# Performance work log

Hardware: AMD Instinct MI355X
Metric: run time of the kernel (lower is better)

The kernel has to match this reference:

```python
import jax, jax.numpy as jnp
import numpy as np
from jax import lax

KH = 5
KW = 5


def dwconv3x3(x, w, b):
    # depthwise 3x3, padding 1; w: (C,1,3,3), b: (C,)
    C = x.shape[1]
    y = lax.conv_general_dilated(x, w, (1, 1), ((1, 1), (1, 1)),
                                 feature_group_count=C,
                                 dimension_numbers=('NCHW', 'OIHW', 'NCHW'))
    return y + b[None, :, None, None]


def conv3x3(x, w, b):
    y = lax.conv_general_dilated(x, w, (1, 1), ((1, 1), (1, 1)),
                                 dimension_numbers=('NCHW', 'OIHW', 'NCHW'))
    return y + b[None, :, None, None]


def resize_bilinear_ac(x, H, W):
    # bilinear, align_corners=True (matches F.interpolate(..., align_corners=True))
    N, C, h, w = x.shape
    ys = jnp.linspace(0.0, h - 1.0, H)
    xs = jnp.linspace(0.0, w - 1.0, W)
    y0 = jnp.floor(ys).astype(jnp.int32)
    x0 = jnp.floor(xs).astype(jnp.int32)
    y1 = jnp.clip(y0 + 1, 0, h - 1)
    x1 = jnp.clip(x0 + 1, 0, w - 1)
    wy = (ys - y0)[None, None, :, None]
    wx = (xs - x0)[None, None, None, :]
    rows = x[:, :, y0, :] * (1.0 - wy) + x[:, :, y1, :] * wy  # (N,C,H,w)
    out = rows[:, :, :, x0] * (1.0 - wx) + rows[:, :, :, x1] * wx  # (N,C,H,W)
    return out


def unfold_kxk(x, kH, kW):
    # torch.nn.Unfold(kernel=(kH,kW), padding=(kH//2,kW//2)) reshaped to (N,C,kH*kW,H,W)
    N, C, H, W = x.shape
    ph, pw = kH // 2, kW // 2
    xp = jnp.pad(x, ((0, 0), (0, 0), (ph, ph), (pw, pw)))
    patches = [xp[:, :, i:i + H, j:j + W] for i in range(kH) for j in range(kW)]
    return jnp.stack(patches, axis=2)  # (N,C,kH*kW,H,W), row-major window order


def setup_inputs() -> dict:
    key = jax.random.key(0)
    ks = jax.random.split(key, 11)
    N, C, H, W = 2, 128, 128, 128
    s = 1.0 / np.sqrt(9.0)
    return {
        'hr_feat': jax.random.normal(ks[0], (N, C, H, W), jnp.float32),
        'lr_feat': jax.random.normal(ks[1], (N, C, H // 2, W // 2), jnp.float32),
        'wq': jax.random.normal(ks[2], (C, 1, 3, 3), jnp.float32) * s,
        'bq': jax.random.normal(ks[3], (C,), jnp.float32) * 0.02,
        'wk': jax.random.normal(ks[4], (C, 1, 3, 3), jnp.float32) * s,
        'bk': jax.random.normal(ks[5], (C,), jnp.float32) * 0.02,
        'wv': jax.random.normal(ks[6], (C, 1, 3, 3), jnp.float32) * s,
        'bv': jax.random.normal(ks[7], (C,), jnp.float32) * 0.02,
        'wa': jax.random.normal(ks[8], (2, 2 * C, 3, 3), jnp.float32) * (1.0 / np.sqrt(9.0 * 2 * C)),
        'ba': jax.random.normal(ks[9], (2,), jnp.float32) * 0.02,
    }


def reference(hr_feat, lr_feat, wq, bq, wk, bk, wv, bv, wa, ba):
    N, C, H, W = hr_feat.shape
    lr_up = resize_bilinear_ac(lr_feat, H, W)
    hr_value = dwconv3x3(hr_feat, wv, bv)
    hr_key = dwconv3x3(hr_feat, wk, bk)
    lr_query = dwconv3x3(lr_up, wq, bq)
    fused = jnp.concatenate([lr_query, hr_key], axis=1)
    dyn = jax.nn.sigmoid(conv3x3(fused, wa, ba))  # (N,2,H,W)
    k_unf = unfold_kxk(hr_key, KH, KW)            # (N,C,K,H,W)
    sim = jnp.einsum('nchw,nckhw->nkhw', lr_query, k_unf)
    weight = jax.nn.softmax(sim, axis=1)          # softmax over window K
    v_unf = unfold_kxk(hr_value, KH, KW)
    attn = dyn[:, 0:1] * jnp.einsum('nckhw,nkhw->nchw', v_unf, weight)
    attn = attn + dyn[:, 1:2] * hr_value
    return lr_up + attn
```

## Files before the change

kernel.cpp:

```cpp
#include <hip/hip_runtime.h>
#include <hip/hip_fp16.h>
#include <math.h>

constexpr int C  = 128;
constexpr int H  = 128;
constexpr int Wd = 128;
constexpr int HW = H * Wd;
constexpr int LH = 64, LW = 64;
constexpr int CP = 64;

constexpr int KRW = 136;
constexpr int KPLANE = 132 * KRW;
constexpr int QRW = 136;
constexpr int QPLANE = 130 * QRW;
constexpr int KSZ = 2 * CP * KPLANE;
constexpr int QSZ = 2 * CP * QPLANE;
constexpr int LSZ = 2 * CP * HW;
constexpr int WAHSZ = 2304;

typedef _Float16 __attribute__((ext_vector_type(2))) v2h;

#if __has_builtin(__builtin_amdgcn_fdot2)
#define DOT2(a, b, c) __builtin_amdgcn_fdot2((a), (b), (c), false)
#else
#define DOT2(a, b, c) ((c) + (float)(a).x * (float)(b).x + (float)(a).y * (float)(b).y)
#endif

struct __attribute__((packed, aligned(4)))  f4u { float x, y, z, w; };
struct __attribute__((packed, aligned(4)))  f4p { v2h a, b, c, d; };
struct __attribute__((packed, aligned(8)))  h2x2 { v2h a, b; };
struct __attribute__((packed, aligned(16))) h4 { v2h a, b, c, d; };

__device__ __forceinline__ v2h pack2(float a, float b) {
  v2h r; r.x = (_Float16)a; r.y = (_Float16)b; return r;
}

__global__ __launch_bounds__(256) void k_pre(
    const float* __restrict__ hr, const float* __restrict__ lr,
    const float* __restrict__ wq, const float* __restrict__ bq,
    const float* __restrict__ wk, const float* __restrict__ bk,
    const float* __restrict__ wv, const float* __restrict__ bv,
    const float* __restrict__ wa,
    v2h* __restrict__ qpad, v2h* __restrict__ kpad, v2h* __restrict__ vpad,
    v2h* __restrict__ lrup, v2h* __restrict__ zgapA, v2h* __restrict__ zgapB,
    v2h* __restrict__ wah)
{
  const int B   = blockIdx.x;
  const int tid = threadIdx.x;
  const int t   = B * 256 + tid;
  const int q   = B & 7;
  const int m   = B >> 3;
  const int j   = (q << 1) | (m & 1);
  const int ncp = m >> 1;
  const int x4  = tid & 31;
  const int y   = (j << 3) | ((tid >> 5) & 7);
  const int x   = x4 * 4;
  const int cp  = ncp & (CP - 1);
  const int n   = ncp >> 6;
  const int c0  = cp * 2;
  const v2h hz  = pack2(0.f, 0.f);
  h4 Z; Z.a = hz; Z.b = hz; Z.c = hz; Z.d = hz;

  if (t < WAHSZ) {
    const int cpw = t / 36, r = t - cpw * 36;
    const int o = r / 18, s2 = (r - o * 18) / 9, tap = r - o * 18 - s2 * 9;
    const int c = s2 * 128 + 2 * cpw;
    wah[t] = pack2(wa[(o * 256 + c) * 9 + tap], wa[(o * 256 + c + 1) * 9 + tap]);
  }

  float ko[2][4], vo[2][4];
#pragma unroll
  for (int cc = 0; cc < 2; cc++) {
    const int c = c0 + cc;
    const float* hp = hr + (n * C + c) * HW;
    const float* wkc = wk + c * 9;
    const float* wvc = wv + c * 9;
    const float bkc = bk[c], bvc = bv[c];
#pragma unroll
    for (int jj = 0; jj < 4; jj++) { ko[cc][jj] = bkc; vo[cc][jj] = bvc; }
#pragma unroll
    for (int r = 0; r < 3; r++) {
      const int gy = y + r - 1;
      const bool okr = (gy >= 0) && (gy < H);
      const int gyc = min(max(gy, 0), H - 1);
      const float* rp = hp + gyc * Wd;
      const f4u mm = *(const f4u*)(rp + x);
      const float lft = rp[max(x - 1, 0)];
      const float rgt = rp[min(x + 4, Wd - 1)];
      float h[6];
      h[0] = (okr && x > 0) ? lft : 0.f;
      h[1] = okr ? mm.x : 0.f;  h[2] = okr ? mm.y : 0.f;
      h[3] = okr ? mm.z : 0.f;  h[4] = okr ? mm.w : 0.f;
      h[5] = (okr && x + 4 < Wd) ? rgt : 0.f;
#pragma unroll
      for (int dj = 0; dj < 3; dj++) {
        const float a = wkc[r * 3 + dj], b = wvc[r * 3 + dj];
#pragma unroll
        for (int jj = 0; jj < 4; jj++) {
          ko[cc][jj] += a * h[jj + dj];
          vo[cc][jj] += b * h[jj + dj];
        }
      }
    }
  }

  v2h* kr = kpad + ncp * KPLANE + (y + 2) * KRW + 4 + x;
  v2h* vr = vpad + ncp * KPLANE + (y + 2) * KRW + 4 + x;
  {
    h4 K4; K4.a = pack2(ko[0][0], ko[1][0]); K4.b = pack2(ko[0][1], ko[1][1]);
           K4.c = pack2(ko[0][2], ko[1][2]); K4.d = pack2(ko[0][3], ko[1][3]);
    h4 V4; V4.a = pack2(vo[0][0], vo[1][0]); V4.b = pack2(vo[0][1], vo[1][1]);
           V4.c = pack2(vo[0][2], vo[1][2]); V4.d = pack2(vo[0][3], vo[1][3]);
    *(h4*)(kr) = K4;
    *(h4*)(vr) = V4;
  }

  const float s = 63.0f / 127.0f;

  float rwm[3][3]; int rA[3];
  {
    int ry0[3]; float wyv[3]; bool okr[3];
#pragma unroll
    for (int r = 0; r < 3; r++) {
      const int gy = y + r - 1;
      okr[r] = (gy >= 0) && (gy < H);
      const int gyc = min(max(gy, 0), H - 1);
      const float fy = gyc * s;
      const int y0 = (int)fy;
      ry0[r] = y0;
      wyv[r] = fy - y0;
    }
    const int Y = ry0[0];
#pragma unroll
    for (int tt = 0; tt < 3; tt++) rA[tt] = min(Y + tt, LH - 1) * LW;
#pragma unroll
    for (int r = 0; r < 3; r++) {
      const int i0 = ry0[r] - Y;
      const int i1 = min(ry0[r] + 1, LH - 1) - Y;
#pragma unroll
      for (int tt = 0; tt < 3; tt++) {
        const float w = ((tt == i0) ? (1.f - wyv[r]) : 0.f)
                      + ((tt == i1) ? wyv[r] : 0.f);
        rwm[r][tt] = okr[r] ? w : 0.f;
      }
    }
  }

  float cwm[6][5]; int XB;
  {
    int cx0[6]; float wxv[6]; bool okc[6];
#pragma unroll
    for (int jj = 0; jj < 6; jj++) {
      const int gx = x + jj - 1;
      okc[jj] = (gx >= 0) && (gx < Wd);
      const int gxc = min(max(gx, 0), Wd - 1);
      const float fx = gxc * s;
      const int x0 = (int)fx;
      cx0[jj] = x0;
      wxv[jj] = fx - x0;
    }
    XB = min(cx0[0], LW - 5);
#pragma unroll
    for (int jj = 0; jj < 6; jj++) {
      const int i0 = cx0[jj] - XB;
      const int i1 = min(cx0[jj] + 1, LW - 1) - XB;
#pragma unroll
      for (int u = 0; u < 5; u++) {
        const float w = ((u == i0) ? (1.f - wxv[jj]) : 0.f)
                      + ((u == i1) ? wxv[jj] : 0.f);
        cwm[jj][u] = okc[jj] ? w : 0.f;
      }
    }
  }

  float qo[2][4], up[2][4];
#pragma unroll
  for (int cc = 0; cc < 2; cc++) {
    const int c = c0 + cc;
    const float* lp = lr + (n * C + c) * (LH * LW);
    const float* wqc = wq + c * 9;
    const float bqc = bq[c];
#pragma unroll
    for (int jj = 0; jj < 4; jj++) qo[cc][jj] = bqc;

    float R[3][5];
#pragma unroll
    for (int tt = 0; tt < 3; tt++) {
      const f4u mm = *(const f4u*)(lp + rA[tt] + XB);
      R[tt][0] = mm.x; R[tt][1] = mm.y; R[tt][2] = mm.z; R[tt][3] = mm.w;
      R[tt][4] = lp[rA[tt] + XB + 4];
    }

    float yi[3][5];
#pragma unroll
    for (int r = 0; r < 3; r++)
#pragma unroll
      for (int u = 0; u < 5; u++)
        yi[r][u] = rwm[r][0] * R[0][u] + rwm[r][1] * R[1][u]
                 + rwm[r][2] * R[2][u];

#pragma unroll
    for (int r = 0; r < 3; r++) {
      float row[6];
#pragma unroll
      for (int jj = 0; jj < 6; jj++)
        row[jj] = cwm[jj][0] * yi[r][0] + cwm[jj][1] * yi[r][1]
               + cwm[jj][2] * yi[r][2] + cwm[jj][3] * yi[r][3]
               + cwm[jj][4] * yi[r][4];
#pragma unroll
      for (int dj = 0; dj < 3; dj++) {
        const float a = wqc[r * 3 + dj];
#pragma unroll
        for (int jj = 0; jj < 4; jj++) qo[cc][jj] += a * row[jj + dj];
      }
      if (r == 1) {
        up[cc][0] = row[1]; up[cc][1] = row[2];
        up[cc][2] = row[3]; up[cc][3] = row[4];
      }
    }
  }

  {
    h4 U;
    U.a = pack2(up[0][0], up[1][0]); U.b = pack2(up[0][1], up[1][1]);
    U.c = pack2(up[0][2], up[1][2]); U.d = pack2(up[0][3], up[1][3]);
    *(h4*)(lrup + ncp * HW + y * Wd + x) = U;
  }
  v2h* qr = qpad + ncp * QPLANE + (y + 1) * QRW + 4 + x;
  {
    h4 Q4; Q4.a = pack2(qo[0][0], qo[1][0]); Q4.b = pack2(qo[0][1], qo[1][1]);
           Q4.c = pack2(qo[0][2], qo[1][2]); Q4.d = pack2(qo[0][3], qo[1][3]);
    *(h4*)(qr) = Q4;
  }

  if (x4 == 0) {
    *(h4*)(kr - 4) = Z; *(h4*)(vr - 4) = Z; *(h4*)(qr - 4) = Z;
  }
  if (x4 == 31) {
    *(h4*)(kr + 4) = Z; *(h4*)(vr + 4) = Z; *(h4*)(qr + 4) = Z;
  }
  if (y == 0) {
    v2h* kz = kpad + ncp * KPLANE;
    v2h* vz = vpad + ncp * KPLANE;
    v2h* qz = qpad + ncp * QPLANE;
    *(h4*)(kz + 4 + x) = Z; *(h4*)(kz + KRW + 4 + x) = Z;
    *(h4*)(vz + 4 + x) = Z; *(h4*)(vz + KRW + 4 + x) = Z;
    *(h4*)(qz + 4 + x) = Z;
    if (x4 == 0) {
      *(h4*)(kz) = Z; *(h4*)(kz + KRW) = Z;
      *(h4*)(vz) = Z; *(h4*)(vz + KRW) = Z;
      *(h4*)(qz) = Z;
    }
    if (x4 == 31) {
      *(h4*)(kz + 132) = Z; *(h4*)(kz + KRW + 132) = Z;
      *(h4*)(vz + 132) = Z; *(h4*)(vz + KRW + 132) = Z;
      *(h4*)(qz + 132) = Z;
    }
  }
  if (y == 127) {
    v2h* kz = kpad + ncp * KPLANE + 130 * KRW;
    v2h* vz = vpad + ncp * KPLANE + 130 * KRW;
    v2h* qz = qpad + ncp * QPLANE + 129 * QRW;
    *(h4*)(kz + 4 + x) = Z; *(h4*)(kz + KRW + 4 + x) = Z;
    *(h4*)(vz + 4 + x) = Z; *(h4*)(vz + KRW + 4 + x) = Z;
    *(h4*)(qz + 4 + x) = Z;
    if (x4 == 0) {
      *(h4*)(kz) = Z; *(h4*)(kz + KRW) = Z;
      *(h4*)(vz) = Z; *(h4*)(vz + KRW) = Z;
      *(h4*)(qz) = Z;
    }
    if (x4 == 31) {
      *(h4*)(kz + 132) = Z; *(h4*)(kz + KRW + 132) = Z;
      *(h4*)(vz + 132) = Z; *(h4*)(vz + KRW + 132) = Z;
      *(h4*)(qz + 132) = Z;
    }
  }
  if (t < 256) zgapA[t] = hz;
  if (t < 4)   zgapB[t] = hz;
}

#define DECLK(P, kp) \
  const f4p P##A0 = *(const f4p*)(kp); \
  const f4p P##A1 = *(const f4p*)((kp) + KRW); \
  const f4p P##A2 = *(const f4p*)((kp) + 2 * KRW); \
  const f4p P##A3 = *(const f4p*)((kp) + 3 * KRW); \
  const f4p P##A4 = *(const f4p*)((kp) + 4 * KRW); \
  const v2h P##b0 = (kp)[4]; \
  const v2h P##b1 = (kp)[KRW + 4]; \
  const v2h P##b2 = (kp)[2 * KRW + 4]; \
  const v2h P##b3 = (kp)[3 * KRW + 4]; \
  const v2h P##b4 = (kp)[4 * KRW + 4];

#define DECLQ(P, qp) \
  const f4p P##Q0 = *(const f4p*)(qp); \
  const f4p P##Q1 = *(const f4p*)((qp) + QRW); \
  const f4p P##Q2 = *(const f4p*)((qp) + 2 * QRW);

#define SIM25(P, qc) \
  sim[0]  = DOT2(qc, P##A0.a, sim[0]);  sim[1]  = DOT2(qc, P##A0.b, sim[1]); \
  sim[2]  = DOT2(qc, P##A0.c, sim[2]);  sim[3]  = DOT2(qc, P##A0.d, sim[3]); \
  sim[4]  = DOT2(qc, P##b0,   sim[4]); \
  sim[5]  = DOT2(qc, P##A1.a, sim[5]);  sim[6]  = DOT2(qc, P##A1.b, sim[6]); \
  sim[7]  = DOT2(qc, P##A1.c, sim[7]);  sim[8]  = DOT2(qc, P##A1.d, sim[8]); \
  sim[9]  = DOT2(qc, P##b1,   sim[9]); \
  sim[10] = DOT2(qc, P##A2.a, sim[10]); sim[11] = DOT2(qc, P##A2.b, sim[11]); \
  sim[12] = DOT2(qc, P##A2.c, sim[12]); sim[13] = DOT2(qc, P##A2.d, sim[13]); \
  sim[14] = DOT2(qc, P##b2,   sim[14]); \
  sim[15] = DOT2(qc, P##A3.a, sim[15]); sim[16] = DOT2(qc, P##A3.b, sim[16]); \
  sim[17] = DOT2(qc, P##A3.c, sim[17]); sim[18] = DOT2(qc, P##A3.d, sim[18]); \
  sim[19] = DOT2(qc, P##b3,   sim[19]); \
  sim[20] = DOT2(qc, P##A4.a, sim[20]); sim[21] = DOT2(qc, P##A4.b, sim[21]); \
  sim[22] = DOT2(qc, P##A4.c, sim[22]); sim[23] = DOT2(qc, P##A4.d, sim[23]); \
  sim[24] = DOT2(qc, P##b4,   sim[24]);

#define GATE(P, wp) { \
  const v2h q3_[9] = {P##Q0.a, P##Q0.b, P##Q0.c, P##Q1.a, P##Q1.b, P##Q1.c, \
                      P##Q2.a, P##Q2.b, P##Q2.c}; \
  const v2h k3_[9] = {P##A1.b, P##A1.c, P##A1.d, P##A2.b, P##A2.c, P##A2.d, \
                      P##A3.b, P##A3.c, P##A3.d}; \
  _Pragma("unroll") \
  for (int tp = 0; tp < 9; tp++) { \
    d0a = DOT2((wp)[tp],      q3_[tp], d0a); \
    d0a = DOT2((wp)[9 + tp],  k3_[tp], d0a); \
    d1a = DOT2((wp)[18 + tp], q3_[tp], d1a); \
    d1a = DOT2((wp)[27 + tp], k3_[tp], d1a); \
  } }

#define EPI(P, ci) { \
  v2h accA = wpk[0] * P##A0.a; \
  accA += wpk[1]  * P##A0.b;  accA += wpk[2]  * P##A0.c; \
  accA += wpk[3]  * P##A0.d;  accA += wpk[4]  * P##b0; \
  v2h accB = wpk[5] * P##A1.a; \
  accB += wpk[6]  * P##A1.b;  accB += wpk[7]  * P##A1.c; \
  accB += wpk[8]  * P##A1.d;  accB += wpk[9]  * P##b1; \
  accA += wpk[10] * P##A2.a;  accA += wpk[11] * P##A2.b; \
  accA += wpk[12] * P##A2.c;  accA += wpk[13] * P##A2.d; \
  accA += wpk[14] * P##b2; \
  accB += wpk[15] * P##A3.a;  accB += wpk[16] * P##A3.b; \
  accB += wpk[17] * P##A3.c;  accB += wpk[18] * P##A3.d; \
  accB += wpk[19] * P##b3; \
  accA += wpk[20] * P##A4.a;  accA += wpk[21] * P##A4.b; \
  accA += wpk[22] * P##A4.c;  accA += wpk[23] * P##A4.d; \
  accA += wpk[24] * P##b4; \
  const float acc0 = (float)accA.x + (float)accB.x; \
  const float acc1 = (float)accA.y + (float)accB.y; \
  const v2h vc = P##A2.c; \
  const v2h lu = lub[(ci) * HW]; \
  float* op = opb + (ci) * 2 * HW; \
  op[0]  = (float)lu.x + g0 * acc0 + g1 * (float)vc.x; \
  op[HW] = (float)lu.y + g0 * acc1 + g1 * (float)vc.y; }

__global__ __launch_bounds__(1024, 4) void k_attn(
    const v2h* __restrict__ qpad, const v2h* __restrict__ kpad,
    const v2h* __restrict__ vpad, const v2h* __restrict__ lrup,
    const v2h* __restrict__ wah, const float* __restrict__ ba,
    float* __restrict__ outb)
{
  __shared__ float red[25 * 1024];
  __shared__ float dsh[2 * 1024];

  const int tid = threadIdx.x;
  const int px  = tid & 63;
  const int cgu = __builtin_amdgcn_readfirstlane((tid >> 6) & 7);
  const int row = __builtin_amdgcn_readfirstlane(tid >> 9);
  const int slot = blockIdx.x;
  const int xcd = slot & 7;
  const int m   = slot >> 3;
  const int y   = (xcd << 4) + ((m & 7) << 1) + row;
  const int x   = ((m >> 3) & 1) * 64 + px;
  const int n   = m >> 4;
  const int cp0 = cgu * 8;

  const float ba0 = ba[0], ba1 = ba[1];

  const v2h* kb = kpad + (n * CP + cp0) * KPLANE + y * KRW + 2 + x;
  const v2h* qb = qpad + (n * CP + cp0) * QPLANE + y * QRW + 3 + x;

  float sim[25];
#pragma unroll
  for (int k = 0; k < 25; k++) sim[k] = 0.f;
  float d0a = 0.f, d1a = 0.f;

#pragma unroll
  for (int cib = 0; cib < 8; cib += 2) {
    const v2h* kp0 = kb + cib * KPLANE;
    const v2h* kp1 = kp0 + KPLANE;
    const v2h* qp0 = qb + cib * QPLANE;
    const v2h* qp1 = qp0 + QPLANE;

    DECLK(S, kp0)
    DECLK(T, kp1)
    DECLQ(S, qp0)

    const v2h qc0 = SQ1.b;
    SIM25(S, qc0)
    GATE(S, wah + (cp0 + cib) * 36)

    DECLQ(T, qp1)
    const v2h qc1 = TQ1.b;
    SIM25(T, qc1)
    GATE(T, wah + (cp0 + cib + 1) * 36)
  }

#pragma unroll
  for (int k = 0; k < 25; k++) red[k * 1024 + tid] = sim[k];
  dsh[tid] = d0a;
  dsh[1024 + tid] = d1a;
  __syncthreads();

  {
    const int w = tid >> 6;
    for (int s = w; s < 54; s += 16) {
      if (s < 50) {
        const int k = s >> 1, r = s & 1;
        float acc = 0.f;
#pragma unroll
        for (int g = 0; g < 8; g++) acc += red[k * 1024 + r * 512 + g * 64 + px];
        red[k * 1024 + r * 512 + px] = acc;
      } else {
        const int jj = s - 50;
        const int r = jj & 1, which = jj >> 1;
        float acc = 0.f;
#pragma unroll
        for (int g = 0; g < 8; g++) acc += dsh[which * 1024 + r * 512 + g * 64 + px];
        dsh[which * 1024 + r * 512 + px] = acc;
      }
    }
  }
  __syncthreads();

  const v2h* vb = vpad + (n * CP + cp0) * KPLANE + y * KRW + 2 + x;
  const v2h* lub = lrup + (n * CP + cp0) * HW + y * Wd + x;
  float* opb = outb + (n * C + 2 * cp0) * HW + y * Wd + x;

  DECLK(VA, vb)
  DECLK(VB, vb + KPLANE)

  const int rbase = row * 512 + px;
  float w[25];
  float mx = -1e30f;
#pragma unroll
  for (int k = 0; k < 25; k++) { w[k] = red[k * 1024 + rbase]; mx = fmaxf(mx, w[k]); }
  float tot = 0.f;
#pragma unroll
  for (int k = 0; k < 25; k++) { const float e = __expf(w[k] - mx); w[k] = e; tot += e; }
  const float inv = __builtin_amdgcn_rcpf(tot);
  v2h wpk[25];
#pragma unroll
  for (int k = 0; k < 25; k++) {
    const float wf = w[k] * inv;
    wpk[k] = pack2(wf, wf);
  }
  const float g0 = __builtin_amdgcn_rcpf(1.f + __expf(-(dsh[rbase] + ba0)));
  const float g1 = __builtin_amdgcn_rcpf(1.f + __expf(-(dsh[1024 + rbase] + ba1)));

  EPI(VA, 0)
  EPI(VB, 1)

#pragma unroll
  for (int cib = 2; cib < 8; cib += 2) {
    DECLK(VC, vb + cib * KPLANE)
    DECLK(VD, vb + (cib + 1) * KPLANE)
    EPI(VC, cib)
    EPI(VD, cib + 1)
  }
}

extern "C" void kernel_launch(void* const* d_in, const int* in_sizes, int n_in,
                              void* d_out, int out_size, void* d_ws,
                              size_t ws_size, hipStream_t stream)
{
  const float* hr = (const float*)d_in[0];
  const float* lr = (const float*)d_in[1];
  const float* wq = (const float*)d_in[2];
  const float* bq = (const float*)d_in[3];
  const float* wk = (const float*)d_in[4];
  const float* bk = (const float*)d_in[5];
  const float* wv = (const float*)d_in[6];
  const float* bv = (const float*)d_in[7];
  const float* wa = (const float*)d_in[8];
  const float* ba = (const float*)d_in[9];

  float* out = (float*)d_out;
  v2h* ws2 = (v2h*)d_ws;

  v2h* kpad  = ws2;
  v2h* vpad  = kpad + KSZ;
  v2h* qpad  = vpad + KSZ;
  v2h* zgapA = qpad + QSZ;
  v2h* lrupb = zgapA + 256;
  v2h* zgapB = lrupb + LSZ;
  v2h* wahb  = zgapB + 4;

  k_pre<<<dim3(2048), dim3(256), 0, stream>>>(
      hr, lr, wq, bq, wk, bk, wv, bv, wa,
      qpad, kpad, vpad, lrupb, zgapA, zgapB, wahb);
  k_attn<<<dim3(256), dim3(1024), 0, stream>>>(
      qpad, kpad, vpad, lrupb, wahb, ba, out);
}
```

Before: 118.1 us.

## Fuse preprocessing and attention kernels into one cooperative launch with grid sync

Merges the k_pre and k_attn kernels into a single cooperative kernel. Each 1024-thread block first computes the q/k/v depthwise convs and the upsampled features for its own tile, then synchronises the whole grid before running the attention stage. This removes one kernel launch and the gap between kernels. In exchange the preprocessing stage now runs on only 256 large blocks instead of 2048 small ones, and the grid-wide barrier has its own cost.

```diff
diff --git a/kernel.cpp b/kernel.cpp
--- a/kernel.cpp
+++ b/kernel.cpp
@@ -1,6 +1,9 @@
 #include <hip/hip_runtime.h>
 #include <hip/hip_fp16.h>
+#include <hip/hip_cooperative_groups.h>
 #include <math.h>
+
+namespace cg = cooperative_groups;
 
 constexpr int C  = 128;
 constexpr int H  = 128;
@@ -28,255 +31,10 @@
 
 struct __attribute__((packed, aligned(4)))  f4u { float x, y, z, w; };
 struct __attribute__((packed, aligned(4)))  f4p { v2h a, b, c, d; };
-struct __attribute__((packed, aligned(8)))  h2x2 { v2h a, b; };
 struct __attribute__((packed, aligned(16))) h4 { v2h a, b, c, d; };
 
 __device__ __forceinline__ v2h pack2(float a, float b) {
   v2h r; r.x = (_Float16)a; r.y = (_Float16)b; return r;
-}
-
-__global__ __launch_bounds__(256) void k_pre(
-    const float* __restrict__ hr, const float* __restrict__ lr,
-    const float* __restrict__ wq, const float* __restrict__ bq,
-    const float* __restrict__ wk, const float* __restrict__ bk,
-    const float* __restrict__ wv, const float* __restrict__ bv,
-    const float* __restrict__ wa,
-    v2h* __restrict__ qpad, v2h* __restrict__ kpad, v2h* __restrict__ vpad,
-    v2h* __restrict__ lrup, v2h* __restrict__ zgapA, v2h* __restrict__ zgapB,
-    v2h* __restrict__ wah)
-{
-  const int B   = blockIdx.x;
-  const int tid = threadIdx.x;
-  const int t   = B * 256 + tid;
-  const int q   = B & 7;
-  const int m   = B >> 3;
-  const int j   = (q << 1) | (m & 1);
-  const int ncp = m >> 1;
-  const int x4  = tid & 31;
-  const int y   = (j << 3) | ((tid >> 5) & 7);
-  const int x   = x4 * 4;
-  const int cp  = ncp & (CP - 1);
-  const int n   = ncp >> 6;
-  const int c0  = cp * 2;
-  const v2h hz  = pack2(0.f, 0.f);
-  h4 Z; Z.a = hz; Z.b = hz; Z.c = hz; Z.d = hz;
-
-  if (t < WAHSZ) {
-    const int cpw = t / 36, r = t - cpw * 36;
-    const int o = r / 18, s2 = (r - o * 18) / 9, tap = r - o * 18 - s2 * 9;
-    const int c = s2 * 128 + 2 * cpw;
-    wah[t] = pack2(wa[(o * 256 + c) * 9 + tap], wa[(o * 256 + c + 1) * 9 + tap]);
-  }
-
-  float ko[2][4], vo[2][4];
-#pragma unroll
-  for (int cc = 0; cc < 2; cc++) {
-    const int c = c0 + cc;
-    const float* hp = hr + (n * C + c) * HW;
-    const float* wkc = wk + c * 9;
-    const float* wvc = wv + c * 9;
-    const float bkc = bk[c], bvc = bv[c];
-#pragma unroll
-    for (int jj = 0; jj < 4; jj++) { ko[cc][jj] = bkc; vo[cc][jj] = bvc; }
-#pragma unroll
-    for (int r = 0; r < 3; r++) {
-      const int gy = y + r - 1;
-      const bool okr = (gy >= 0) && (gy < H);
-      const int gyc = min(max(gy, 0), H - 1);
-      const float* rp = hp + gyc * Wd;
-      const f4u mm = *(const f4u*)(rp + x);
-      const float lft = rp[max(x - 1, 0)];
-      const float rgt = rp[min(x + 4, Wd - 1)];
-      float h[6];
-      h[0] = (okr && x > 0) ? lft : 0.f;
-      h[1] = okr ? mm.x : 0.f;  h[2] = okr ? mm.y : 0.f;
-      h[3] = okr ? mm.z : 0.f;  h[4] = okr ? mm.w : 0.f;
-      h[5] = (okr && x + 4 < Wd) ? rgt : 0.f;
-#pragma unroll
-      for (int dj = 0; dj < 3; dj++) {
-        const float a = wkc[r * 3 + dj], b = wvc[r * 3 + dj];
-#pragma unroll
-        for (int jj = 0; jj < 4; jj++) {
-          ko[cc][jj] += a * h[jj + dj];
-          vo[cc][jj] += b * h[jj + dj];
-        }
-      }
-    }
-  }
-
-  v2h* kr = kpad + ncp * KPLANE + (y + 2) * KRW + 4 + x;
-  v2h* vr = vpad + ncp * KPLANE + (y + 2) * KRW + 4 + x;
-  {
-    h4 K4; K4.a = pack2(ko[0][0], ko[1][0]); K4.b = pack2(ko[0][1], ko[1][1]);
-           K4.c = pack2(ko[0][2], ko[1][2]); K4.d = pack2(ko[0][3], ko[1][3]);
-    h4 V4; V4.a = pack2(vo[0][0], vo[1][0]); V4.b = pack2(vo[0][1], vo[1][1]);
-           V4.c = pack2(vo[0][2], vo[1][2]); V4.d = pack2(vo[0][3], vo[1][3]);
-    *(h4*)(kr) = K4;
-    *(h4*)(vr) = V4;
-  }
-
-  const float s = 63.0f / 127.0f;
-
-  float rwm[3][3]; int rA[3];
-  {
-    int ry0[3]; float wyv[3]; bool okr[3];
-#pragma unroll
-    for (int r = 0; r < 3; r++) {
-      const int gy = y + r - 1;
-      okr[r] = (gy >= 0) && (gy < H);
-      const int gyc = min(max(gy, 0), H - 1);
-      const float fy = gyc * s;
-      const int y0 = (int)fy;
-      ry0[r] = y0;
-      wyv[r] = fy - y0;
-    }
-    const int Y = ry0[0];
-#pragma unroll
-    for (int tt = 0; tt < 3; tt++) rA[tt] = min(Y + tt, LH - 1) * LW;
-#pragma unroll
-    for (int r = 0; r < 3; r++) {
-      const int i0 = ry0[r] - Y;
-      const int i1 = min(ry0[r] + 1, LH - 1) - Y;
-#pragma unroll
-      for (int tt = 0; tt < 3; tt++) {
-        const float w = ((tt == i0) ? (1.f - wyv[r]) : 0.f)
-                      + ((tt == i1) ? wyv[r] : 0.f);
-        rwm[r][tt] = okr[r] ? w : 0.f;
-      }
-    }
-  }
-
-  float cwm[6][5]; int XB;
-  {
-    int cx0[6]; float wxv[6]; bool okc[6];
-#pragma unroll
-    for (int jj = 0; jj < 6; jj++) {
-      const int gx = x + jj - 1;
-      okc[jj] = (gx >= 0) && (gx < Wd);
-      const int gxc = min(max(gx, 0), Wd - 1);
-      const float fx = gxc * s;
-      const int x0 = (int)fx;
-      cx0[jj] = x0;
-      wxv[jj] = fx - x0;
-    }
-    XB = min(cx0[0], LW - 5);
-#pragma unroll
-    for (int jj = 0; jj < 6; jj++) {
-      const int i0 = cx0[jj] - XB;
-      const int i1 = min(cx0[jj] + 1, LW - 1) - XB;
-#pragma unroll
-      for (int u = 0; u < 5; u++) {
-        const float w = ((u == i0) ? (1.f - wxv[jj]) : 0.f)
-                      + ((u == i1) ? wxv[jj] : 0.f);
-        cwm[jj][u] = okc[jj] ? w : 0.f;
-      }
-    }
-  }
-
-  float qo[2][4], up[2][4];
-#pragma unroll
-  for (int cc = 0; cc < 2; cc++) {
-    const int c = c0 + cc;
-    const float* lp = lr + (n * C + c) * (LH * LW);
-    const float* wqc = wq + c * 9;
-    const float bqc = bq[c];
-#pragma unroll
-    for (int jj = 0; jj < 4; jj++) qo[cc][jj] = bqc;
-
-    float R[3][5];
-#pragma unroll
-    for (int tt = 0; tt < 3; tt++) {
-      const f4u mm = *(const f4u*)(lp + rA[tt] + XB);
-      R[tt][0] = mm.x; R[tt][1] = mm.y; R[tt][2] = mm.z; R[tt][3] = mm.w;
-      R[tt][4] = lp[rA[tt] + XB + 4];
-    }
-
-    float yi[3][5];
-#pragma unroll
-    for (int r = 0; r < 3; r++)
-#pragma unroll
-      for (int u = 0; u < 5; u++)
-        yi[r][u] = rwm[r][0] * R[0][u] + rwm[r][1] * R[1][u]
-                 + rwm[r][2] * R[2][u];
-
-#pragma unroll
-    for (int r = 0; r < 3; r++) {
-      float row[6];
-#pragma unroll
-      for (int jj = 0; jj < 6; jj++)
-        row[jj] = cwm[jj][0] * yi[r][0] + cwm[jj][1] * yi[r][1]
-               + cwm[jj][2] * yi[r][2] + cwm[jj][3] * yi[r][3]
-               + cwm[jj][4] * yi[r][4];
-#pragma unroll
-      for (int dj = 0; dj < 3; dj++) {
-        const float a = wqc[r * 3 + dj];
-#pragma unroll
-        for (int jj = 0; jj < 4; jj++) qo[cc][jj] += a * row[jj + dj];
-      }
-      if (r == 1) {
-        up[cc][0] = row[1]; up[cc][1] = row[2];
-        up[cc][2] = row[3]; up[cc][3] = row[4];
-      }
-    }
-  }
-
-  {
-    h4 U;
-    U.a = pack2(up[0][0], up[1][0]); U.b = pack2(up[0][1], up[1][1]);
-    U.c = pack2(up[0][2], up[1][2]); U.d = pack2(up[0][3], up[1][3]);
-    *(h4*)(lrup + ncp * HW + y * Wd + x) = U;
-  }
-  v2h* qr = qpad + ncp * QPLANE + (y + 1) * QRW + 4 + x;
-  {
-    h4 Q4; Q4.a = pack2(qo[0][0], qo[1][0]); Q4.b = pack2(qo[0][1], qo[1][1]);
-           Q4.c = pack2(qo[0][2], qo[1][2]); Q4.d = pack2(qo[0][3], qo[1][3]);
-    *(h4*)(qr) = Q4;
-  }
-
-  if (x4 == 0) {
-    *(h4*)(kr - 4) = Z; *(h4*)(vr - 4) = Z; *(h4*)(qr - 4) = Z;
-  }
-  if (x4 == 31) {
-    *(h4*)(kr + 4) = Z; *(h4*)(vr + 4) = Z; *(h4*)(qr + 4) = Z;
-  }
-  if (y == 0) {
-    v2h* kz = kpad + ncp * KPLANE;
-    v2h* vz = vpad + ncp * KPLANE;
-    v2h* qz = qpad + ncp * QPLANE;
-    *(h4*)(kz + 4 + x) = Z; *(h4*)(kz + KRW + 4 + x) = Z;
-    *(h4*)(vz + 4 + x) = Z; *(h4*)(vz + KRW + 4 + x) = Z;
-    *(h4*)(qz + 4 + x) = Z;
-    if (x4 == 0) {
-      *(h4*)(kz) = Z; *(h4*)(kz + KRW) = Z;
-      *(h4*)(vz) = Z; *(h4*)(vz + KRW) = Z;
-      *(h4*)(qz) = Z;
-    }
-    if (x4 == 31) {
-      *(h4*)(kz + 132) = Z; *(h4*)(kz + KRW + 132) = Z;
-      *(h4*)(vz + 132) = Z; *(h4*)(vz + KRW + 132) = Z;
-      *(h4*)(qz + 132) = Z;
-    }
-  }
-  if (y == 127) {
-    v2h* kz = kpad + ncp * KPLANE + 130 * KRW;
-    v2h* vz = vpad + ncp * KPLANE + 130 * KRW;
-    v2h* qz = qpad + ncp * QPLANE + 129 * QRW;
-    *(h4*)(kz + 4 + x) = Z; *(h4*)(kz + KRW + 4 + x) = Z;
-    *(h4*)(vz + 4 + x) = Z; *(h4*)(vz + KRW + 4 + x) = Z;
-    *(h4*)(qz + 4 + x) = Z;
-    if (x4 == 0) {
-      *(h4*)(kz) = Z; *(h4*)(kz + KRW) = Z;
-      *(h4*)(vz) = Z; *(h4*)(vz + KRW) = Z;
-      *(h4*)(qz) = Z;
-    }
-    if (x4 == 31) {
-      *(h4*)(kz + 132) = Z; *(h4*)(kz + KRW + 132) = Z;
-      *(h4*)(vz + 132) = Z; *(h4*)(vz + KRW + 132) = Z;
-      *(h4*)(qz + 132) = Z;
-    }
-  }
-  if (t < 256) zgapA[t] = hz;
-  if (t < 4)   zgapB[t] = hz;
 }
 
 #define DECLK(P, kp) \
@@ -350,119 +108,359 @@
   op[0]  = (float)lu.x + g0 * acc0 + g1 * (float)vc.x; \
   op[HW] = (float)lu.y + g0 * acc1 + g1 * (float)vc.y; }
 
-__global__ __launch_bounds__(1024, 4) void k_attn(
-    const v2h* __restrict__ qpad, const v2h* __restrict__ kpad,
-    const v2h* __restrict__ vpad, const v2h* __restrict__ lrup,
-    const v2h* __restrict__ wah, const float* __restrict__ ba,
-    float* __restrict__ outb)
+__global__ __launch_bounds__(1024, 4) void k_fused(
+    const float* __restrict__ hr, const float* __restrict__ lr,
+    const float* __restrict__ wq, const float* __restrict__ bq,
+    const float* __restrict__ wk, const float* __restrict__ bk,
+    const float* __restrict__ wv, const float* __restrict__ bv,
+    const float* __restrict__ wa, const float* __restrict__ ba,
+    v2h* __restrict__ qpad, v2h* __restrict__ kpad, v2h* __restrict__ vpad,
+    v2h* __restrict__ lrup, v2h* __restrict__ zgapA, v2h* __restrict__ zgapB,
+    v2h* __restrict__ wah, float* __restrict__ outb)
 {
   __shared__ float red[25 * 1024];
   __shared__ float dsh[2 * 1024];
 
-  const int tid = threadIdx.x;
-  const int px  = tid & 63;
-  const int cgu = __builtin_amdgcn_readfirstlane((tid >> 6) & 7);
-  const int row = __builtin_amdgcn_readfirstlane(tid >> 9);
+  const int tid  = threadIdx.x;
   const int slot = blockIdx.x;
-  const int xcd = slot & 7;
-  const int m   = slot >> 3;
-  const int y   = (xcd << 4) + ((m & 7) << 1) + row;
-  const int x   = ((m >> 3) & 1) * 64 + px;
-  const int n   = m >> 4;
-  const int cp0 = cgu * 8;
-
-  const float ba0 = ba[0], ba1 = ba[1];
-
-  const v2h* kb = kpad + (n * CP + cp0) * KPLANE + y * KRW + 2 + x;
-  const v2h* qb = qpad + (n * CP + cp0) * QPLANE + y * QRW + 3 + x;
-
-  float sim[25];
-#pragma unroll
-  for (int k = 0; k < 25; k++) sim[k] = 0.f;
-  float d0a = 0.f, d1a = 0.f;
-
-#pragma unroll
-  for (int cib = 0; cib < 8; cib += 2) {
-    const v2h* kp0 = kb + cib * KPLANE;
-    const v2h* kp1 = kp0 + KPLANE;
-    const v2h* qp0 = qb + cib * QPLANE;
-    const v2h* qp1 = qp0 + QPLANE;
-
-    DECLK(S, kp0)
-    DECLK(T, kp1)
-    DECLQ(S, qp0)
-
-    const v2h qc0 = SQ1.b;
-    SIM25(S, qc0)
-    GATE(S, wah + (cp0 + cib) * 36)
-
-    DECLQ(T, qp1)
-    const v2h qc1 = TQ1.b;
-    SIM25(T, qc1)
-    GATE(T, wah + (cp0 + cib + 1) * 36)
-  }
-
-#pragma unroll
-  for (int k = 0; k < 25; k++) red[k * 1024 + tid] = sim[k];
-  dsh[tid] = d0a;
-  dsh[1024 + tid] = d1a;
-  __syncthreads();
+  const int xcd  = slot & 7;
+  const int mm_  = slot >> 3;
+  const int y0   = (xcd << 4) + ((mm_ & 7) << 1);
+  const int x0   = ((mm_ >> 3) & 1) * 64;
+  const int n    = mm_ >> 4;
 
   {
-    const int w = tid >> 6;
-    for (int s = w; s < 54; s += 16) {
-      if (s < 50) {
-        const int k = s >> 1, r = s & 1;
-        float acc = 0.f;
-#pragma unroll
-        for (int g = 0; g < 8; g++) acc += red[k * 1024 + r * 512 + g * 64 + px];
-        red[k * 1024 + r * 512 + px] = acc;
-      } else {
-        const int jj = s - 50;
-        const int r = jj & 1, which = jj >> 1;
-        float acc = 0.f;
-#pragma unroll
-        for (int g = 0; g < 8; g++) acc += dsh[which * 1024 + r * 512 + g * 64 + px];
-        dsh[which * 1024 + r * 512 + px] = acc;
+    const int cp  = tid >> 4;
+    const int xq  = tid & 15;
+    const int xx  = x0 + xq * 4;
+    const int ncp = n * CP + cp;
+    const int c0  = cp * 2;
+    const v2h hz  = pack2(0.f, 0.f);
+    h4 Z; Z.a = hz; Z.b = hz; Z.c = hz; Z.d = hz;
+    const float s = 63.0f / 127.0f;
+
+    if (slot == 0) {
+      for (int t = tid; t < WAHSZ; t += 1024) {
+        const int cpw = t / 36, r = t - cpw * 36;
+        const int o = r / 18, s2 = (r - o * 18) / 9, tap = r - o * 18 - s2 * 9;
+        const int c = s2 * 128 + 2 * cpw;
+        wah[t] = pack2(wa[(o * 256 + c) * 9 + tap], wa[(o * 256 + c + 1) * 9 + tap]);
+      }
+      if (tid < 256) zgapA[tid] = hz;
+      if (tid < 4)   zgapB[tid] = hz;
+    }
+
+#pragma unroll
+    for (int r2 = 0; r2 < 2; r2++) {
+      const int yy = y0 + r2;
+
+      float ko[2][4], vo[2][4];
+#pragma unroll
+      for (int cc = 0; cc < 2; cc++) {
+        const int c = c0 + cc;
+        const float* hp = hr + (n * C + c) * HW;
+        const float* wkc = wk + c * 9;
+        const float* wvc = wv + c * 9;
+        const float bkc = bk[c], bvc = bv[c];
+#pragma unroll
+        for (int jj = 0; jj < 4; jj++) { ko[cc][jj] = bkc; vo[cc][jj] = bvc; }
+#pragma unroll
+        for (int r = 0; r < 3; r++) {
+          const int gy = yy + r - 1;
+          const bool okr = (gy >= 0) && (gy < H);
+          const int gyc = min(max(gy, 0), H - 1);
+          const float* rp = hp + gyc * Wd;
+          const f4u mv = *(const f4u*)(rp + xx);
+          const float lft = rp[max(xx - 1, 0)];
+          const float rgt = rp[min(xx + 4, Wd - 1)];
+          float h[6];
+          h[0] = (okr && xx > 0) ? lft : 0.f;
+          h[1] = okr ? mv.x : 0.f;  h[2] = okr ? mv.y : 0.f;
+          h[3] = okr ? mv.z : 0.f;  h[4] = okr ? mv.w : 0.f;
+          h[5] = (okr && xx + 4 < Wd) ? rgt : 0.f;
+#pragma unroll
+          for (int dj = 0; dj < 3; dj++) {
+            const float a = wkc[r * 3 + dj], b = wvc[r * 3 + dj];
+#pragma unroll
+            for (int jj = 0; jj < 4; jj++) {
+              ko[cc][jj] += a * h[jj + dj];
+              vo[cc][jj] += b * h[jj + dj];
+            }
+          }
+        }
+      }
+
+      v2h* kr = kpad + ncp * KPLANE + (yy + 2) * KRW + 4 + xx;
+      v2h* vr = vpad + ncp * KPLANE + (yy + 2) * KRW + 4 + xx;
+      {
+        h4 K4; K4.a = pack2(ko[0][0], ko[1][0]); K4.b = pack2(ko[0][1], ko[1][1]);
+               K4.c = pack2(ko[0][2], ko[1][2]); K4.d = pack2(ko[0][3], ko[1][3]);
+        h4 V4; V4.a = pack2(vo[0][0], vo[1][0]); V4.b = pack2(vo[0][1], vo[1][1]);
+               V4.c = pack2(vo[0][2], vo[1][2]); V4.d = pack2(vo[0][3], vo[1][3]);
+        *(h4*)(kr) = K4;
+        *(h4*)(vr) = V4;
+      }
+
+      float rwm[3][3]; int rA[3];
+      {
+        int ry0[3]; float wyv[3]; bool okr[3];
+#pragma unroll
+        for (int r = 0; r < 3; r++) {
+          const int gy = yy + r - 1;
+          okr[r] = (gy >= 0) && (gy < H);
+          const int gyc = min(max(gy, 0), H - 1);
+          const float fy = gyc * s;
+          const int yb = (int)fy;
+          ry0[r] = yb;
+          wyv[r] = fy - yb;
+        }
+        const int Y = ry0[0];
+#pragma unroll
+        for (int tt = 0; tt < 3; tt++) rA[tt] = min(Y + tt, LH - 1) * LW;
+#pragma unroll
+        for (int r = 0; r < 3; r++) {
+          const int i0 = ry0[r] - Y;
+          const int i1 = min(ry0[r] + 1, LH - 1) - Y;
+#pragma unroll
+          for (int tt = 0; tt < 3; tt++) {
+            const float w = ((tt == i0) ? (1.f - wyv[r]) : 0.f)
+                          + ((tt == i1) ? wyv[r] : 0.f);
+            rwm[r][tt] = okr[r] ? w : 0.f;
+          }
+        }
+      }
+
+      float cwm[6][5]; int XB;
+      {
+        int cx0[6]; float wxv[6]; bool okc[6];
+#pragma unroll
+        for (int jj = 0; jj < 6; jj++) {
+          const int gx = xx + jj - 1;
+          okc[jj] = (gx >= 0) && (gx < Wd);
+          const int gxc = min(max(gx, 0), Wd - 1);
+          const float fx = gxc * s;
+          const int xb = (int)fx;
+          cx0[jj] = xb;
+          wxv[jj] = fx - xb;
+        }
+        XB = min(cx0[0], LW - 5);
+#pragma unroll
+        for (int jj = 0; jj < 6; jj++) {
+          const int i0 = cx0[jj] - XB;
+          const int i1 = min(cx0[jj] + 1, LW - 1) - XB;
+#pragma unroll
+          for (int u = 0; u < 5; u++) {
+            const float w = ((u == i0) ? (1.f - wxv[jj]) : 0.f)
+                          + ((u == i1) ? wxv[jj] : 0.f);
+            cwm[jj][u] = okc[jj] ? w : 0.f;
+          }
+        }
+      }
+
+      float qo[2][4], up[2][4];
+#pragma unroll
+      for (int cc = 0; cc < 2; cc++) {
+        const int c = c0 + cc;
+        const float* lp = lr + (n * C + c) * (LH * LW);
+        const float* wqc = wq + c * 9;
+        const float bqc = bq[c];
+#pragma unroll
+        for (int jj = 0; jj < 4; jj++) qo[cc][jj] = bqc;
+
+        float R[3][5];
+#pragma unroll
+        for (int tt = 0; tt < 3; tt++) {
+          const f4u mv = *(const f4u*)(lp + rA[tt] + XB);
+          R[tt][0] = mv.x; R[tt][1] = mv.y; R[tt][2] = mv.z; R[tt][3] = mv.w;
+          R[tt][4] = lp[rA[tt] + XB + 4];
+        }
+
+        float yi[3][5];
+#pragma unroll
+        for (int r = 0; r < 3; r++)
+#pragma unroll
+          for (int u = 0; u < 5; u++)
+            yi[r][u] = rwm[r][0] * R[0][u] + rwm[r][1] * R[1][u]
+                     + rwm[r][2] * R[2][u];
+
+#pragma unroll
+        for (int r = 0; r < 3; r++) {
+          float rowv[6];
+#pragma unroll
+          for (int jj = 0; jj < 6; jj++)
+            rowv[jj] = cwm[jj][0] * yi[r][0] + cwm[jj][1] * yi[r][1]
+                     + cwm[jj][2] * yi[r][2] + cwm[jj][3] * yi[r][3]
+                     + cwm[jj][4] * yi[r][4];
+#pragma unroll
+          for (int dj = 0; dj < 3; dj++) {
+            const float a = wqc[r * 3 + dj];
+#pragma unroll
+            for (int jj = 0; jj < 4; jj++) qo[cc][jj] += a * rowv[jj + dj];
+          }
+          if (r == 1) {
+            up[cc][0] = rowv[1]; up[cc][1] = rowv[2];
+            up[cc][2] = rowv[3]; up[cc][3] = rowv[4];
+          }
+        }
+      }
+
+      {
+        h4 U;
+        U.a = pack2(up[0][0], up[1][0]); U.b = pack2(up[0][1], up[1][1]);
+        U.c = pack2(up[0][2], up[1][2]); U.d = pack2(up[0][3], up[1][3]);
+        *(h4*)(lrup + ncp * HW + yy * Wd + xx) = U;
+      }
+      v2h* qr = qpad + ncp * QPLANE + (yy + 1) * QRW + 4 + xx;
+      {
+        h4 Q4; Q4.a = pack2(qo[0][0], qo[1][0]); Q4.b = pack2(qo[0][1], qo[1][1]);
+               Q4.c = pack2(qo[0][2], qo[1][2]); Q4.d = pack2(qo[0][3], qo[1][3]);
+        *(h4*)(qr) = Q4;
+      }
+
+      if (xx == 0)   { *(h4*)(kr - 4) = Z; *(h4*)(vr - 4) = Z; *(h4*)(qr - 4) = Z; }
+      if (xx == 124) { *(h4*)(kr + 4) = Z; *(h4*)(vr + 4) = Z; *(h4*)(qr + 4) = Z; }
+      if (yy == 0) {
+        v2h* kz = kpad + ncp * KPLANE;
+        v2h* vz = vpad + ncp * KPLANE;
+        v2h* qz = qpad + ncp * QPLANE;
+        *(h4*)(kz + 4 + xx) = Z; *(h4*)(kz + KRW + 4 + xx) = Z;
+        *(h4*)(vz + 4 + xx) = Z; *(h4*)(vz + KRW + 4 + xx) = Z;
+        *(h4*)(qz + 4 + xx) = Z;
+        if (xx == 0) {
+          *(h4*)(kz) = Z; *(h4*)(kz + KRW) = Z;
+          *(h4*)(vz) = Z; *(h4*)(vz + KRW) = Z;
+          *(h4*)(qz) = Z;
+        }
+        if (xx == 124) {
+          *(h4*)(kz + 132) = Z; *(h4*)(kz + KRW + 132) = Z;
+          *(h4*)(vz + 132) = Z; *(h4*)(vz + KRW + 132) = Z;
+          *(h4*)(qz + 132) = Z;
+        }
+      }
+      if (yy == 127) {
+        v2h* kz = kpad + ncp * KPLANE + 130 * KRW;
+        v2h* vz = vpad + ncp * KPLANE + 130 * KRW;
+        v2h* qz = qpad + ncp * QPLANE + 129 * QRW;
+        *(h4*)(kz + 4 + xx) = Z; *(h4*)(kz + KRW + 4 + xx) = Z;
+        *(h4*)(vz + 4 + xx) = Z; *(h4*)(vz + KRW + 4 + xx) = Z;
+        *(h4*)(qz + 4 + xx) = Z;
+        if (xx == 0) {
+          *(h4*)(kz) = Z; *(h4*)(kz + KRW) = Z;
+          *(h4*)(vz) = Z; *(h4*)(vz + KRW) = Z;
+          *(h4*)(qz) = Z;
+        }
+        if (xx == 124) {
+          *(h4*)(kz + 132) = Z; *(h4*)(kz + KRW + 132) = Z;
+          *(h4*)(vz + 132) = Z; *(h4*)(vz + KRW + 132) = Z;
+          *(h4*)(qz + 132) = Z;
+        }
       }
     }
   }
-  __syncthreads();
-
-  const v2h* vb = vpad + (n * CP + cp0) * KPLANE + y * KRW + 2 + x;
-  const v2h* lub = lrup + (n * CP + cp0) * HW + y * Wd + x;
-  float* opb = outb + (n * C + 2 * cp0) * HW + y * Wd + x;
-
-  DECLK(VA, vb)
-  DECLK(VB, vb + KPLANE)
-
-  const int rbase = row * 512 + px;
-  float w[25];
-  float mx = -1e30f;
-#pragma unroll
-  for (int k = 0; k < 25; k++) { w[k] = red[k * 1024 + rbase]; mx = fmaxf(mx, w[k]); }
-  float tot = 0.f;
-#pragma unroll
-  for (int k = 0; k < 25; k++) { const float e = __expf(w[k] - mx); w[k] = e; tot += e; }
-  const float inv = __builtin_amdgcn_rcpf(tot);
-  v2h wpk[25];
-#pragma unroll
-  for (int k = 0; k < 25; k++) {
-    const float wf = w[k] * inv;
-    wpk[k] = pack2(wf, wf);
-  }
-  const float g0 = __builtin_amdgcn_rcpf(1.f + __expf(-(dsh[rbase] + ba0)));
-  const float g1 = __builtin_amdgcn_rcpf(1.f + __expf(-(dsh[1024 + rbase] + ba1)));
-
-  EPI(VA, 0)
-  EPI(VB, 1)
-
-#pragma unroll
-  for (int cib = 2; cib < 8; cib += 2) {
-    DECLK(VC, vb + cib * KPLANE)
-    DECLK(VD, vb + (cib + 1) * KPLANE)
-    EPI(VC, cib)
-    EPI(VD, cib + 1)
+
+  cg::this_grid().sync();
+
+  {
+    const int px  = tid & 63;
+    const int cgu = __builtin_amdgcn_readfirstlane((tid >> 6) & 7);
+    const int row = __builtin_amdgcn_readfirstlane(tid >> 9);
+    const int y   = y0 + row;
+    const int x   = x0 + px;
+    const int cp0 = cgu * 8;
+
+    const float ba0 = ba[0], ba1 = ba[1];
+
+    const v2h* kb = kpad + (n * CP + cp0) * KPLANE + y * KRW + 2 + x;
+    const v2h* qb = qpad + (n * CP + cp0) * QPLANE + y * QRW + 3 + x;
+
+    float sim[25];
+#pragma unroll
+    for (int k = 0; k < 25; k++) sim[k] = 0.f;
+    float d0a = 0.f, d1a = 0.f;
+
+#pragma unroll
+    for (int cib = 0; cib < 8; cib += 2) {
+      const v2h* kp0 = kb + cib * KPLANE;
+      const v2h* kp1 = kp0 + KPLANE;
+      const v2h* qp0 = qb + cib * QPLANE;
+      const v2h* qp1 = qp0 + QPLANE;
+
+      DECLK(S, kp0)
+      DECLK(T, kp1)
+      DECLQ(S, qp0)
+
+      const v2h qc0 = SQ1.b;
+      SIM25(S, qc0)
+      GATE(S, wah + (cp0 + cib) * 36)
+
+      DECLQ(T, qp1)
+      const v2h qc1 = TQ1.b;
+      SIM25(T, qc1)
+      GATE(T, wah + (cp0 + cib + 1) * 36)
+    }
+
+#pragma unroll
+    for (int k = 0; k < 25; k++) red[k * 1024 + tid] = sim[k];
+    dsh[tid] = d0a;
+    dsh[1024 + tid] = d1a;
+    __syncthreads();
+
+    {
+      const int w = tid >> 6;
+      for (int sjob = w; sjob < 54; sjob += 16) {
+        if (sjob < 50) {
+          const int k = sjob >> 1, r = sjob & 1;
+          float acc = 0.f;
+#pragma unroll
+          for (int g = 0; g < 8; g++) acc += red[k * 1024 + r * 512 + g * 64 + px];
+          red[k * 1024 + r * 512 + px] = acc;
+        } else {
+          const int jj = sjob - 50;
+          const int r = jj & 1, which = jj >> 1;
+          float acc = 0.f;
+#pragma unroll
+          for (int g = 0; g < 8; g++) acc += dsh[which * 1024 + r * 512 + g * 64 + px];
+          dsh[which * 1024 + r * 512 + px] = acc;
+        }
+      }
+    }
+    __syncthreads();
+
+    const v2h* vb = vpad + (n * CP + cp0) * KPLANE + y * KRW + 2 + x;
+    const v2h* lub = lrup + (n * CP + cp0) * HW + y * Wd + x;
+    float* opb = outb + (n * C + 2 * cp0) * HW + y * Wd + x;
+
+    DECLK(VA, vb)
+    DECLK(VB, vb + KPLANE)
+
+    const int rbase = row * 512 + px;
+    float w[25];
+    float mx = -1e30f;
+#pragma unroll
+    for (int k = 0; k < 25; k++) { w[k] = red[k * 1024 + rbase]; mx = fmaxf(mx, w[k]); }
+    float tot = 0.f;
+#pragma unroll
+    for (int k = 0; k < 25; k++) { const float e = __expf(w[k] - mx); w[k] = e; tot += e; }
+    const float inv = __builtin_amdgcn_rcpf(tot);
+    v2h wpk[25];
+#pragma unroll
+    for (int k = 0; k < 25; k++) {
+      const float wf = w[k] * inv;
+      wpk[k] = pack2(wf, wf);
+    }
+    const float g0 = __builtin_amdgcn_rcpf(1.f + __expf(-(dsh[rbase] + ba0)));
+    const float g1 = __builtin_amdgcn_rcpf(1.f + __expf(-(dsh[1024 + rbase] + ba1)));
+
+    EPI(VA, 0)
+    EPI(VB, 1)
+
+#pragma unroll
+    for (int cib = 2; cib < 8; cib += 2) {
+      DECLK(VC, vb + cib * KPLANE)
+      DECLK(VD, vb + (cib + 1) * KPLANE)
+      EPI(VC, cib)
+      EPI(VD, cib + 1)
+    }
   }
 }
 
@@ -492,9 +490,12 @@
   v2h* zgapB = lrupb + LSZ;
   v2h* wahb  = zgapB + 4;
 
-  k_pre<<<dim3(2048), dim3(256), 0, stream>>>(
-      hr, lr, wq, bq, wk, bk, wv, bv, wa,
-      qpad, kpad, vpad, lrupb, zgapA, zgapB, wahb);
-  k_attn<<<dim3(256), dim3(1024), 0, stream>>>(
-      qpad, kpad, vpad, lrupb, wahb, ba, out);
+  void* args[] = {
+    (void*)&hr, (void*)&lr, (void*)&wq, (void*)&bq, (void*)&wk, (void*)&bk,
+    (void*)&wv, (void*)&bv, (void*)&wa, (void*)&ba,
+    (void*)&qpad, (void*)&kpad, (void*)&vpad, (void*)&lrupb,
+    (void*)&zgapA, (void*)&zgapB, (void*)&wahb, (void*)&out
+  };
+  hipLaunchCooperativeKernel((const void*)k_fused, dim3(256), dim3(1024),
+                             args, 0, stream);
 }
```

Result: slower. 229.8 us (+94.6%).

## Split attention block to one row with LDS atomic channel reduction

Applied to the files above, without the earlier changes.

Each k_attn block now covers one row of 64 pixels instead of two, with 16 wavefronts each handling 4 channel pairs instead of 8. The grid doubles to 512 blocks. The two-phase shared-memory tree reduction over 25+2 floats per thread is replaced by LDS atomicAdd into a small 27x64 buffer, which shrinks LDS use so more blocks can be resident; launch bounds are raised accordingly. The intent is more parallelism and occupancy with less LDS traffic, at the cost of LDS atomic contention (16 waves hitting the same addresses) and a nondeterministic float summation order.

```diff
diff --git a/kernel.cpp b/kernel.cpp
--- a/kernel.cpp
+++ b/kernel.cpp
@@ -28,7 +28,6 @@
 
 struct __attribute__((packed, aligned(4)))  f4u { float x, y, z, w; };
 struct __attribute__((packed, aligned(4)))  f4p { v2h a, b, c, d; };
-struct __attribute__((packed, aligned(8)))  h2x2 { v2h a, b; };
 struct __attribute__((packed, aligned(16))) h4 { v2h a, b, c, d; };
 
 __device__ __forceinline__ v2h pack2(float a, float b) {
@@ -350,28 +349,29 @@
   op[0]  = (float)lu.x + g0 * acc0 + g1 * (float)vc.x; \
   op[HW] = (float)lu.y + g0 * acc1 + g1 * (float)vc.y; }
 
-__global__ __launch_bounds__(1024, 4) void k_attn(
+__global__ __launch_bounds__(1024, 8) void k_attn(
     const v2h* __restrict__ qpad, const v2h* __restrict__ kpad,
     const v2h* __restrict__ vpad, const v2h* __restrict__ lrup,
     const v2h* __restrict__ wah, const float* __restrict__ ba,
     float* __restrict__ outb)
 {
-  __shared__ float red[25 * 1024];
-  __shared__ float dsh[2 * 1024];
+  __shared__ float accd[27 * 64];
 
   const int tid = threadIdx.x;
   const int px  = tid & 63;
-  const int cgu = __builtin_amdgcn_readfirstlane((tid >> 6) & 7);
-  const int row = __builtin_amdgcn_readfirstlane(tid >> 9);
+  const int cgu = __builtin_amdgcn_readfirstlane(tid >> 6);
   const int slot = blockIdx.x;
   const int xcd = slot & 7;
   const int m   = slot >> 3;
-  const int y   = (xcd << 4) + ((m & 7) << 1) + row;
-  const int x   = ((m >> 3) & 1) * 64 + px;
-  const int n   = m >> 4;
-  const int cp0 = cgu * 8;
+  const int y   = (xcd << 4) | (m & 15);
+  const int x   = ((m >> 4) & 1) * 64 + px;
+  const int n   = m >> 5;
+  const int cp0 = cgu * 4;
 
   const float ba0 = ba[0], ba1 = ba[1];
+
+  for (int i = tid; i < 27 * 64; i += 1024) accd[i] = 0.f;
+  __syncthreads();
 
   const v2h* kb = kpad + (n * CP + cp0) * KPLANE + y * KRW + 2 + x;
   const v2h* qb = qpad + (n * CP + cp0) * QPLANE + y * QRW + 3 + x;
@@ -382,51 +382,20 @@
   float d0a = 0.f, d1a = 0.f;
 
 #pragma unroll
-  for (int cib = 0; cib < 8; cib += 2) {
+  for (int cib = 0; cib < 4; cib++) {
     const v2h* kp0 = kb + cib * KPLANE;
-    const v2h* kp1 = kp0 + KPLANE;
     const v2h* qp0 = qb + cib * QPLANE;
-    const v2h* qp1 = qp0 + QPLANE;
-
     DECLK(S, kp0)
-    DECLK(T, kp1)
     DECLQ(S, qp0)
-
     const v2h qc0 = SQ1.b;
     SIM25(S, qc0)
     GATE(S, wah + (cp0 + cib) * 36)
-
-    DECLQ(T, qp1)
-    const v2h qc1 = TQ1.b;
-    SIM25(T, qc1)
-    GATE(T, wah + (cp0 + cib + 1) * 36)
-  }
-
-#pragma unroll
-  for (int k = 0; k < 25; k++) red[k * 1024 + tid] = sim[k];
-  dsh[tid] = d0a;
-  dsh[1024 + tid] = d1a;
-  __syncthreads();
-
-  {
-    const int w = tid >> 6;
-    for (int s = w; s < 54; s += 16) {
-      if (s < 50) {
-        const int k = s >> 1, r = s & 1;
-        float acc = 0.f;
-#pragma unroll
-        for (int g = 0; g < 8; g++) acc += red[k * 1024 + r * 512 + g * 64 + px];
-        red[k * 1024 + r * 512 + px] = acc;
-      } else {
-        const int jj = s - 50;
-        const int r = jj & 1, which = jj >> 1;
-        float acc = 0.f;
-#pragma unroll
-        for (int g = 0; g < 8; g++) acc += dsh[which * 1024 + r * 512 + g * 64 + px];
-        dsh[which * 1024 + r * 512 + px] = acc;
-      }
-    }
-  }
+  }
+
+#pragma unroll
+  for (int k = 0; k < 25; k++) atomicAdd(&accd[k * 64 + px], sim[k]);
+  atomicAdd(&accd[25 * 64 + px], d0a);
+  atomicAdd(&accd[26 * 64 + px], d1a);
   __syncthreads();
 
   const v2h* vb = vpad + (n * CP + cp0) * KPLANE + y * KRW + 2 + x;
@@ -434,13 +403,11 @@
   float* opb = outb + (n * C + 2 * cp0) * HW + y * Wd + x;
 
   DECLK(VA, vb)
-  DECLK(VB, vb + KPLANE)
-
-  const int rbase = row * 512 + px;
+
   float w[25];
   float mx = -1e30f;
 #pragma unroll
-  for (int k = 0; k < 25; k++) { w[k] = red[k * 1024 + rbase]; mx = fmaxf(mx, w[k]); }
+  for (int k = 0; k < 25; k++) { w[k] = accd[k * 64 + px]; mx = fmaxf(mx, w[k]); }
   float tot = 0.f;
 #pragma unroll
   for (int k = 0; k < 25; k++) { const float e = __expf(w[k] - mx); w[k] = e; tot += e; }
@@ -451,18 +418,15 @@
     const float wf = w[k] * inv;
     wpk[k] = pack2(wf, wf);
   }
-  const float g0 = __builtin_amdgcn_rcpf(1.f + __expf(-(dsh[rbase] + ba0)));
-  const float g1 = __builtin_amdgcn_rcpf(1.f + __expf(-(dsh[1024 + rbase] + ba1)));
+  const float g0 = __builtin_amdgcn_rcpf(1.f + __expf(-(accd[25 * 64 + px] + ba0)));
+  const float g1 = __builtin_amdgcn_rcpf(1.f + __expf(-(accd[26 * 64 + px] + ba1)));
 
   EPI(VA, 0)
-  EPI(VB, 1)
-
-#pragma unroll
-  for (int cib = 2; cib < 8; cib += 2) {
+
+#pragma unroll
+  for (int cib = 1; cib < 4; cib++) {
     DECLK(VC, vb + cib * KPLANE)
-    DECLK(VD, vb + (cib + 1) * KPLANE)
     EPI(VC, cib)
-    EPI(VD, cib + 1)
   }
 }
 
@@ -495,6 +459,6 @@
   k_pre<<<dim3(2048), dim3(256), 0, stream>>>(
       hr, lr, wq, bq, wk, bk, wv, bv, wa,
       qpad, kpad, vpad, lrupb, zgapA, zgapB, wahb);
-  k_attn<<<dim3(256), dim3(1024), 0, stream>>>(
+  k_attn<<<dim3(512), dim3(1024), 0, stream>>>(
       qpad, kpad, vpad, lrupb, wahb, ba, out);
 }
```

After: 186.2 us. 57.6% more time.
